# Performance work log

Hardware: AMD Instinct MI355X
Metric: run time of the kernel (lower is better)

The kernel has to match this reference:

```python
import jax, jax.numpy as jnp
import numpy as np
from jax.scipy.linalg import expm

B, S, D, E, K, NROT = 2, 2048, 1024, 8, 2, 3
EPS = 1e-5


def setup_inputs() -> dict:
    key = jax.random.key(0)
    ks = jax.random.split(key, 16)
    sc = 0.02
    x = jax.random.normal(ks[0], (B, S, D), jnp.float32)
    ln_gamma = 1.0 + sc * jax.random.normal(ks[1], (D,), jnp.float32)
    ln_beta = sc * jax.random.normal(ks[2], (D,), jnp.float32)
    abel_w = sc * jax.random.normal(ks[3], (D, D), jnp.float32)
    abel_b = sc * jax.random.normal(ks[4], (D,), jnp.float32)
    moe_gate_w = sc * jax.random.normal(ks[5], (D, E), jnp.float32)
    moe_gate_b = sc * jax.random.normal(ks[6], (E,), jnp.float32)
    ew1 = sc * jax.random.normal(ks[7], (E, D, 2 * D), jnp.float32)
    eb1 = sc * jax.random.normal(ks[8], (E, 2 * D), jnp.float32)
    ew2 = sc * jax.random.normal(ks[9], (E, 2 * D, D), jnp.float32)
    eb2 = sc * jax.random.normal(ks[10], (E, D), jnp.float32)
    g = sc * jax.random.normal(ks[11], (NROT, D, D), jnp.float32)
    gens = 0.5 * (g - jnp.swapaxes(g, -1, -2))  # skew-symmetric, as in reset_parameters
    gc_w = sc * jax.random.normal(ks[12], (2 * D, 1), jnp.float32)
    gc_b = sc * jax.random.normal(ks[13], (1,), jnp.float32)
    return dict(x=x, ln_gamma=ln_gamma, ln_beta=ln_beta, abel_w=abel_w, abel_b=abel_b,
                moe_gate_w=moe_gate_w, moe_gate_b=moe_gate_b, ew1=ew1, eb1=eb1,
                ew2=ew2, eb2=eb2, gens=gens, gc_w=gc_w, gc_b=gc_b)


def _gelu(x):
    return jax.nn.gelu(x, approximate=False)  # torch nn.GELU default = exact erf


def _forward(x, ln_gamma, ln_beta, abel_w, abel_b, moe_gate_w, moe_gate_b,
             ew1, eb1, ew2, eb2, gens, gc_w, gc_b):
    residual = x
    # LayerNorm
    mu = jnp.mean(x, axis=-1, keepdims=True)
    var = jnp.mean((x - mu) ** 2, axis=-1, keepdims=True)
    xn = (x - mu) * jax.lax.rsqrt(var + EPS) * ln_gamma + ln_beta
    # abel branch: Linear + GELU
    abel_out = _gelu(xn @ abel_w + abel_b)
    # MoE: dense all-experts compute, masked by top-k softmax weights
    logits = xn @ moe_gate_w + moe_gate_b                      # [B,S,E]
    topw, topi = jax.lax.top_k(logits, K)                      # [B,S,K]
    topw = jax.nn.softmax(topw, axis=-1)
    w_dense = jnp.sum(jax.nn.one_hot(topi, E, dtype=xn.dtype) * topw[..., None], axis=-2)  # [B,S,E]
    h = _gelu(jnp.einsum('bsd,edh->ebsh', xn, ew1) + eb1[:, None, None, :])  # [E,B,S,2D]
    eo = jnp.einsum('ebsh,ehd->ebsd', h, ew2) + eb2[:, None, None, :]        # [E,B,S,D]
    moe_out = jnp.einsum('ebsd,bse->bsd', eo, w_dense)
    # GeometricRotation: sequential matrix_exp rotations
    for i in range(NROT):
        moe_out = moe_out @ expm(gens[i])
    # gated residual mix
    combined = jnp.concatenate([abel_out, moe_out], axis=-1)
    gate = jax.nn.sigmoid(combined @ gc_w + gc_b)              # [B,S,1]
    mixed = abel_out * (1.0 - gate) + moe_out * gate
    return residual + mixed


def reference(x, ln_gamma, ln_beta, abel_w, abel_b, moe_gate_w, moe_gate_b,
              ew1, eb1, ew2, eb2, gens, gc_w, gc_b):
    return _forward(x, ln_gamma, ln_beta, abel_w, abel_b, moe_gate_w, moe_gate_b,
                    ew1, eb1, ew2, eb2, gens, gc_w, gc_b)
```

## Files before the change

kernel.cpp:

```cpp
#include <hip/hip_runtime.h>
#include <hip/hip_bf16.h>
#include <cstdint>
#include <cstddef>

#define DD   1024
#define DD2  2048
#define EE   8
#define NTOK 4096
#define CAPR 9216
#define MAXT 72

typedef __bf16 bf16_t;
typedef __bf16 bf16x8 __attribute__((ext_vector_type(8)));
typedef __bf16 bf16x4 __attribute__((ext_vector_type(4)));
typedef float  f32x4v __attribute__((ext_vector_type(4)));

__device__ __forceinline__ float gelu_f(float v){
  const float t = v*(0.7978845608028654f + 0.0356774081f*v*v);
  const float u = __expf(2.0f*t);
  return __fdividef(v*u, 1.0f + u);
}

__device__ __forceinline__ void gload_lds16(const void* g, void* l){
  __builtin_amdgcn_global_load_lds(
    (const __attribute__((address_space(1))) unsigned int*)(uintptr_t)g,
    (__attribute__((address_space(3))) unsigned int*)(uintptr_t)l,
    16, 0, 0);
}

enum { EPI_GELU_F32=0, EPI_GELU_BF16=1, EPI_BIAS_BF16=2, EPI_SCALE_BF16=3,
       EPI_ADDV_BF16=4, EPI_BF16=5, EPI_F32=6 };

template<int BM,int BN,int EPI,bool TAB>
__global__ __launch_bounds__(256)
void gemm_bt(const bf16_t* __restrict__ A, const bf16_t* __restrict__ Bt,
             const int N, const int K, const int gx, const int gy, const int gz,
             const long sAz, const long sBz, const long sOz,
             const int* __restrict__ tileE, const int* __restrict__ tileR,
             const int* __restrict__ ntp, const int* __restrict__ offp,
             const float* __restrict__ bias, const long sBias,
             const float alpha,
             const bf16_t* __restrict__ addv,
             float* __restrict__ outF, bf16_t* __restrict__ outB)
{
  constexpr int BK = 64;
  constexpr int WM = BM/2, WN = BN/2;
  constexpr int FM = WM/16, FN = WN/16;
  constexpr int IA = BM/32, IB = BN/32;
  __shared__ alignas(16) bf16_t sA[2][BM*BK];
  __shared__ alignas(16) bf16_t sB[2][BN*BK];

  int bx, by, bz;
  if constexpr (TAB) {
    const int nwg = gx * gy;
    const int q = nwg >> 3, r = nwg & 7;
    const int k = blockIdx.x & 7, i = blockIdx.x >> 3;
    if (i >= q + (k < r ? 1 : 0)) return;
    const int l = k * q + (k < r ? k : r) + i;
    const int ti = l / gx; bx = l - ti*gx;
    if (ti >= ntp[0]) return;
    bz = tileE[ti];
    by = 0;
    const long ro = (long)offp[bz] + tileR[ti];
    A    += ro * (long)K;
    outB += ro * (long)N;
  } else {
    const int nwg = gx * gy * gz;
    const int q = nwg >> 3, r = nwg & 7;
    const int k = blockIdx.x & 7, i = blockIdx.x >> 3;
    if (i >= q + (k < r ? 1 : 0)) return;
    const int l = k * q + (k < r ? k : r) + i;
    bx = l % gx; const int t2 = l / gx; by = t2 % gy; bz = t2 / gy;
  }

  const int z = bz;
  const bf16_t* Bp = Bt + (size_t)z * sBz;
  float*  oF = outF;
  bf16_t* oB = outB;
  if constexpr (!TAB) {
    A += (size_t)z * sAz;
    if (oF) oF += (size_t)z * sOz;
    if (oB) oB += (size_t)z * sOz;
  }
  const float*  bp = bias ? bias + (size_t)z * sBias : nullptr;
  const bf16_t* vp = addv ? addv + (size_t)z * sOz   : nullptr;

  const int tid = threadIdx.x;
  const int wid = tid >> 6, lid = tid & 63;
  const int wr = wid >> 1, wc = wid & 1;
  const int brow = by * BM, bcol = bx * BN;
  const int sr = lid >> 3, sq = lid & 7;
  const int fr = lid & 15, fq = lid >> 4;

  f32x4v acc[FM][FN] = {};

  auto stage = [&](int buf, int kt) {
    #pragma unroll
    for (int i = 0; i < IA; i++) {
      const int ii = wid*IA + i;
      const int r  = ii*8 + sr;
      const int q  = sq ^ (r & 7);
      gload_lds16((const char*)A + ((size_t)(brow + r)*K + kt)*2 + q*16,
                  (char*)sA[buf] + ii*1024);
    }
    #pragma unroll
    for (int i = 0; i < IB; i++) {
      const int ii = wid*IB + i;
      const int r  = ii*8 + sr;
      const int q  = sq ^ (r & 7);
      gload_lds16((const char*)Bp + ((size_t)(bcol + r)*K + kt)*2 + q*16,
                  (char*)sB[buf] + ii*1024);
    }
  };

  stage(0, 0);
  __syncthreads();
  int cur = 0;

  for (int kt = 0; kt < K; kt += BK) {
    if (kt + BK < K) stage(cur ^ 1, kt + BK);
    #pragma unroll
    for (int kk = 0; kk < 2; kk++) {
      bf16x8 af[FM], bb[FN];
      #pragma unroll
      for (int mi = 0; mi < FM; mi++) {
        const int r = wr*WM + mi*16 + fr;
        const int q = (kk*4 + fq) ^ (r & 7);
        af[mi] = *(const bf16x8*)((const char*)sA[cur] + r*128 + q*16);
      }
      #pragma unroll
      for (int ni = 0; ni < FN; ni++) {
        const int r = wc*WN + ni*16 + fr;
        const int q = (kk*4 + fq) ^ (r & 7);
        bb[ni] = *(const bf16x8*)((const char*)sB[cur] + r*128 + q*16);
      }
      #pragma unroll
      for (int mi = 0; mi < FM; mi++)
        #pragma unroll
        for (int ni = 0; ni < FN; ni++)
          acc[mi][ni] = __builtin_amdgcn_mfma_f32_16x16x32_bf16(
              af[mi], bb[ni], acc[mi][ni], 0, 0, 0);
    }
    __syncthreads();
    cur ^= 1;
  }

  #pragma unroll
  for (int mi = 0; mi < FM; mi++) {
    #pragma unroll
    for (int ni = 0; ni < FN; ni++) {
      const int rg0 = brow + wr*WM + mi*16 + fq*4;
      const int cg  = bcol + wc*WN + ni*16 + fr;
      #pragma unroll
      for (int i = 0; i < 4; i++) {
        const int rg = rg0 + i;
        float v = acc[mi][ni][i];
        if constexpr (EPI == EPI_GELU_F32) {
          v += bp[cg];
          oF[(size_t)rg*N + cg] = gelu_f(v);
        } else if constexpr (EPI == EPI_GELU_BF16) {
          v += bp[cg];
          oB[(size_t)rg*N + cg] = (bf16_t)gelu_f(v);
        } else if constexpr (EPI == EPI_BIAS_BF16) {
          v += bp[cg];
          oB[(size_t)rg*N + cg] = (bf16_t)v;
        } else if constexpr (EPI == EPI_SCALE_BF16) {
          oB[(size_t)rg*N + cg] = (bf16_t)(v * alpha);
        } else if constexpr (EPI == EPI_ADDV_BF16) {
          oB[(size_t)rg*N + cg] = (bf16_t)(v + (float)vp[(size_t)rg*N + cg]);
        } else if constexpr (EPI == EPI_BF16) {
          oB[(size_t)rg*N + cg] = (bf16_t)v;
        } else {
          oF[(size_t)rg*N + cg] = v;
        }
      }
    }
  }
}

__global__ __launch_bounds__(256)
void tcvt_kernel(const float* __restrict__ src, bf16_t* __restrict__ dst, int R, int C){
  __shared__ float t[64][65];
  const size_t bo = (size_t)blockIdx.z * R * C;
  const int c0 = blockIdx.x*64, r0 = blockIdx.y*64;
  const int lx = threadIdx.x & 15, ly = threadIdx.x >> 4;
  #pragma unroll
  for (int i = 0; i < 4; i++) {
    const int row = r0 + ly + i*16;
    const float4 v = *(const float4*)(src + bo + (size_t)row*C + c0 + lx*4);
    t[ly + i*16][lx*4+0] = v.x; t[ly + i*16][lx*4+1] = v.y;
    t[ly + i*16][lx*4+2] = v.z; t[ly + i*16][lx*4+3] = v.w;
  }
  __syncthreads();
  #pragma unroll
  for (int i = 0; i < 4; i++) {
    const int c = c0 + ly + i*16;
    bf16x4 o;
    #pragma unroll
    for (int j = 0; j < 4; j++) o[j] = (bf16_t)t[lx*4+j][ly + i*16];
    *(bf16x4*)(dst + bo + (size_t)c*R + r0 + lx*4) = o;
  }
}

__global__ __launch_bounds__(256)
void tb16_kernel(const bf16_t* __restrict__ Ut, bf16_t* __restrict__ Tb){
  __shared__ bf16_t tile[32][33];
  const bf16_t* src = Ut + (size_t)(1 - blockIdx.z) * DD * DD;
  bf16_t*       dst = Tb + (size_t)blockIdx.z * DD * DD;
  const int c0 = blockIdx.x*32, r0 = blockIdx.y*32;
  #pragma unroll
  for (int i = 0; i < 4; i++)
    tile[threadIdx.y + i*8][threadIdx.x] = src[(size_t)(r0 + threadIdx.y + i*8)*DD + c0 + threadIdx.x];
  __syncthreads();
  #pragma unroll
  for (int i = 0; i < 4; i++)
    dst[(size_t)(c0 + threadIdx.y + i*8)*DD + r0 + threadIdx.x] = tile[threadIdx.x][threadIdx.y + i*8];
}

__global__ __launch_bounds__(256)
void cvt_kernel(const float* __restrict__ in, bf16_t* __restrict__ o, long n, float scale){
  const long i = ((long)blockIdx.x*256 + threadIdx.x)*4;
  if (i >= n) return;
  const float4 v = *(const float4*)(in + i);
  bf16x4 b; b[0]=(bf16_t)(v.x*scale); b[1]=(bf16_t)(v.y*scale);
  b[2]=(bf16_t)(v.z*scale); b[3]=(bf16_t)(v.w*scale);
  *(bf16x4*)(o + i) = b;
}

__global__ __launch_bounds__(256)
void vw_kernel(const bf16_t* __restrict__ Hn, const bf16_t* __restrict__ H2,
               bf16_t* __restrict__ Vb, bf16_t* __restrict__ Wtb){
  const long i0 = ((long)blockIdx.x*256 + threadIdx.x)*4;
  const long rc = i0 % (long)(DD*DD);
  const int r = (int)(rc / DD), c0 = (int)(rc % DD);
  const bf16x4 h  = *(const bf16x4*)(Hn + i0);
  const bf16x4 h2 = *(const bf16x4*)(H2 + i0);
  bf16x4 v, w;
  #pragma unroll
  for (int j = 0; j < 4; j++) {
    const float d  = (r == c0 + j) ? 1.0f : 0.0f;
    const float fh = (float)h[j], f2 = (float)h2[j];
    v[j] = (bf16_t)(d + fh + f2*0.5f);
    w[j] = (bf16_t)(d*(1.0f/6.0f) - fh*(1.0f/24.0f) + f2*(1.0f/120.0f));
  }
  *(bf16x4*)(Vb  + i0) = v;
  *(bf16x4*)(Wtb + i0) = w;
}

__global__ __launch_bounds__(256)
void ln_gate_kernel(const float* __restrict__ x, const float* __restrict__ gamma,
                    const float* __restrict__ beta, const float* __restrict__ gw,
                    const float* __restrict__ gb,
                    bf16_t* __restrict__ xnb, int2* __restrict__ ids,
                    float2* __restrict__ wts)
{
  const int t = blockIdx.x, tid = threadIdx.x, j0 = tid*4;
  const int wid = tid >> 6, lid = tid & 63;
  const float4 v = *(const float4*)(x + (size_t)t*DD + j0);
  float s  = v.x + v.y + v.z + v.w;
  float ss = v.x*v.x + v.y*v.y + v.z*v.z + v.w*v.w;
  #pragma unroll
  for (int off = 32; off; off >>= 1) { s += __shfl_down(s, off); ss += __shfl_down(ss, off); }
  __shared__ float redS[4], redQ[4], mv[2];
  if (lid == 0) { redS[wid] = s; redQ[wid] = ss; }
  __syncthreads();
  if (tid == 0) {
    const float S1 = redS[0]+redS[1]+redS[2]+redS[3];
    const float S2 = redQ[0]+redQ[1]+redQ[2]+redQ[3];
    const float mu  = S1 * (1.0f/DD);
    const float var = S2 * (1.0f/DD) - mu*mu;
    mv[0] = mu; mv[1] = rsqrtf(var + 1e-5f);
  }
  __syncthreads();
  const float mu = mv[0], rstd = mv[1];
  const float4 g = *(const float4*)(gamma + j0);
  const float4 b = *(const float4*)(beta  + j0);
  float xn[4];
  xn[0] = (v.x-mu)*rstd*g.x + b.x;
  xn[1] = (v.y-mu)*rstd*g.y + b.y;
  xn[2] = (v.z-mu)*rstd*g.z + b.z;
  xn[3] = (v.w-mu)*rstd*g.w + b.w;
  bf16x4 ov; ov[0]=(bf16_t)xn[0]; ov[1]=(bf16_t)xn[1]; ov[2]=(bf16_t)xn[2]; ov[3]=(bf16_t)xn[3];
  *(bf16x4*)(xnb + (size_t)t*DD + j0) = ov;

  float p[8] = {0,0,0,0,0,0,0,0};
  #pragma unroll
  for (int i = 0; i < 4; i++) {
    const float4 a0 = *(const float4*)(gw + (size_t)(j0+i)*EE);
    const float4 a1 = *(const float4*)(gw + (size_t)(j0+i)*EE + 4);
    const float xv = xn[i];
    p[0]+=xv*a0.x; p[1]+=xv*a0.y; p[2]+=xv*a0.z; p[3]+=xv*a0.w;
    p[4]+=xv*a1.x; p[5]+=xv*a1.y; p[6]+=xv*a1.z; p[7]+=xv*a1.w;
  }
  #pragma unroll
  for (int off = 32; off; off >>= 1) {
    #pragma unroll
    for (int e = 0; e < 8; e++) p[e] += __shfl_down(p[e], off);
  }
  __shared__ float pr[32];
  if (lid == 0) {
    #pragma unroll
    for (int e = 0; e < 8; e++) pr[wid*8 + e] = p[e];
  }
  __syncthreads();
  if (tid == 0) {
    float l[8];
    #pragma unroll
    for (int e = 0; e < 8; e++) l[e] = pr[e] + pr[8+e] + pr[16+e] + pr[24+e] + gb[e];
    int i1 = 0; float m1 = l[0];
    #pragma unroll
    for (int e = 1; e < 8; e++) if (l[e] > m1) { m1 = l[e]; i1 = e; }
    int i2 = 0; float m2 = -1e30f;
    #pragma unroll
    for (int e = 0; e < 8; e++) if (e != i1 && l[e] > m2) { m2 = l[e]; i2 = e; }
    const float wa = 1.0f/(1.0f + expf(m2 - m1));
    ids[t] = make_int2(i1, i2);
    wts[t] = make_float2(wa, 1.0f - wa);
  }
}

__global__ __launch_bounds__(256)
void route_kernel(const int2* __restrict__ ids, int* __restrict__ slotA,
                  int* __restrict__ slotB, int* __restrict__ cnt,
                  int* __restrict__ off, int* __restrict__ tileE,
                  int* __restrict__ tileR, int* __restrict__ ntp)
{
  const int tid = threadIdx.x;
  const int wid = tid >> 6, lid = tid & 63;
  __shared__ int wsum[EE][4];
  __shared__ int base[EE];
  if (tid < EE) base[tid] = 0;
  __syncthreads();
  const unsigned long long lt = (1ull << lid) - 1ull;
  for (int c0 = 0; c0 < NTOK; c0 += 256) {
    const int t = c0 + tid;
    const int2 id = ids[t];
    int pA = 0, pB = 0;
    #pragma unroll
    for (int e = 0; e < EE; e++) {
      const bool fA = (id.x == e), fB = (id.y == e);
      const unsigned long long mA = __ballot(fA);
      const unsigned long long mB = __ballot(fB);
      const int cA = __popcll(mA);
      if (lid == 0) wsum[e][wid] = cA + __popcll(mB);
      if (fA) pA = __popcll(mA & lt);
      if (fB) pB = cA + __popcll(mB & lt);
    }
    __syncthreads();
    int wbA = base[id.x], wbB = base[id.y];
    for (int w = 0; w < wid; w++) { wbA += wsum[id.x][w]; wbB += wsum[id.y][w]; }
    slotA[t] = wbA + pA;
    slotB[t] = wbB + pB;
    __syncthreads();
    if (tid < EE) base[tid] += wsum[tid][0]+wsum[tid][1]+wsum[tid][2]+wsum[tid][3];
    __syncthreads();
  }
  if (tid == 0) {
    int a = 0, nt = 0;
    for (int e = 0; e < EE; e++) {
      cnt[e] = base[e]; off[e] = a;
      for (int r2 = 0; r2 < base[e]; r2 += 128) { tileE[nt] = e; tileR[nt] = r2; nt++; }
      a += (base[e] + 127) & ~127;
    }
    ntp[0] = nt;
  }
}

__global__ __launch_bounds__(256)
void gather_kernel(const bf16_t* __restrict__ xnb, const int2* __restrict__ ids,
                   const int* __restrict__ slotA, const int* __restrict__ slotB,
                   const int* __restrict__ off, bf16_t* __restrict__ Xg){
  const int t = blockIdx.x, j = threadIdx.x*4;
  const int2 id = ids[t];
  const bf16x4 v = *(const bf16x4*)(xnb + (size_t)t*DD + j);
  *(bf16x4*)(Xg + (size_t)(off[id.x] + slotA[t])*DD + j) = v;
  *(bf16x4*)(Xg + (size_t)(off[id.y] + slotB[t])*DD + j) = v;
}

__global__ __launch_bounds__(256)
void combine_kernel(const bf16_t* __restrict__ Yg, const int2* __restrict__ ids,
                    const int* __restrict__ slotA, const int* __restrict__ slotB,
                    const int* __restrict__ off, const float2* __restrict__ wts,
                    bf16_t* __restrict__ Xa){
  const int t = blockIdx.x, j = threadIdx.x*4;
  const int2 id = ids[t];
  const float2 w = wts[t];
  const bf16x4 a = *(const bf16x4*)(Yg + (size_t)(off[id.x] + slotA[t])*DD + j);
  const bf16x4 b = *(const bf16x4*)(Yg + (size_t)(off[id.y] + slotB[t])*DD + j);
  bf16x4 o;
  #pragma unroll
  for (int i = 0; i < 4; i++) o[i] = (bf16_t)(w.x*(float)a[i] + w.y*(float)b[i]);
  *(bf16x4*)(Xa + (size_t)t*DD + j) = o;
}

__global__ __launch_bounds__(256)
void mix_kernel(const float* __restrict__ x, const bf16_t* __restrict__ abel,
                const float* __restrict__ rot, const float* __restrict__ gcw,
                const float* __restrict__ gcb, float* __restrict__ out)
{
  const int t = blockIdx.x, tid = threadIdx.x, j0 = tid*4;
  const int wid = tid >> 6, lid = tid & 63;
  const bf16x4 ab = *(const bf16x4*)(abel + (size_t)t*DD + j0);
  const float4 r  = *(const float4*)(rot  + (size_t)t*DD + j0);
  const float4 ga = *(const float4*)(gcw + j0);
  const float4 gr = *(const float4*)(gcw + DD + j0);
  const float a0 = (float)ab[0], a1 = (float)ab[1], a2 = (float)ab[2], a3 = (float)ab[3];
  float p = a0*ga.x + a1*ga.y + a2*ga.z + a3*ga.w
          + r.x*gr.x + r.y*gr.y + r.z*gr.z + r.w*gr.w;
  #pragma unroll
  for (int off = 32; off; off >>= 1) p += __shfl_down(p, off);
  __shared__ float red[4];
  __shared__ float gsh;
  if (lid == 0) red[wid] = p;
  __syncthreads();
  if (tid == 0) {
    const float P = red[0] + red[1] + red[2] + red[3] + gcb[0];
    gsh = 1.0f/(1.0f + expf(-P));
  }
  __syncthreads();
  const float gate = gsh, g1 = 1.0f - gate;
  const float4 xv = *(const float4*)(x + (size_t)t*DD + j0);
  float4 o;
  o.x = xv.x + a0*g1 + r.x*gate;
  o.y = xv.y + a1*g1 + r.y*gate;
  o.z = xv.z + a2*g1 + r.z*gate;
  o.w = xv.w + a3*g1 + r.w*gate;
  *(float4*)(out + (size_t)t*DD + j0) = o;
}

extern "C" void kernel_launch(void* const* d_in, const int* in_sizes, int n_in,
                              void* d_out, int out_size, void* d_ws, size_t ws_size,
                              hipStream_t stream)
{
  (void)in_sizes; (void)n_in; (void)out_size; (void)ws_size;
  const float* x      = (const float*)d_in[0];
  const float* ln_g   = (const float*)d_in[1];
  const float* ln_b   = (const float*)d_in[2];
  const float* abel_w = (const float*)d_in[3];
  const float* abel_b = (const float*)d_in[4];
  const float* gate_w = (const float*)d_in[5];
  const float* gate_b = (const float*)d_in[6];
  const float* ew1    = (const float*)d_in[7];
  const float* eb1    = (const float*)d_in[8];
  const float* ew2    = (const float*)d_in[9];
  const float* eb2    = (const float*)d_in[10];
  const float* gens   = (const float*)d_in[11];
  const float* gc_w   = (const float*)d_in[12];
  const float* gc_b   = (const float*)d_in[13];
  float* out = (float*)d_out;

  char* wsp = (char*)d_ws;
  auto alloc = [&](size_t bytes) -> char* {
    char* p = wsp; wsp += (bytes + 255) & ~(size_t)255; return p;
  };
  const size_t MB = 1u<<20;
  bf16_t* xnb   = (bf16_t*)alloc((size_t)NTOK*DD*2);
  int2*   ids   = (int2*)  alloc((size_t)NTOK*8);
  float2* wts   = (float2*)alloc((size_t)NTOK*8);
  int*    slotA = (int*)   alloc((size_t)NTOK*4);
  int*    slotB = (int*)   alloc((size_t)NTOK*4);
  int*    cnt   = (int*)   alloc(64);
  int*    off   = (int*)   alloc(64);
  int*    tileE = (int*)   alloc(MAXT*4);
  int*    tileR = (int*)   alloc(MAXT*4);
  int*    ntp   = (int*)   alloc(64);
  bf16_t* abel_wT = (bf16_t*)alloc((size_t)DD*DD*2);
  char*   UN      = alloc(64*MB);
  bf16_t* ew1T  = (bf16_t*)UN;
  bf16_t* ew2T  = (bf16_t*)(UN + 32*MB);
  bf16_t* Hn    = (bf16_t*)alloc((size_t)3*DD*DD*2);
  bf16_t* abelo = (bf16_t*)alloc((size_t)NTOK*DD*2);
  bf16_t* Xg    = (bf16_t*)alloc((size_t)CAPR*DD*2);
  bf16_t* Hg    = (bf16_t*)alloc((size_t)CAPR*DD2*2);
  bf16_t* Xa    = (bf16_t*)alloc((size_t)NTOK*DD*2);
  bf16_t* Yg    = Xg;
  float*  rot   = (float*)Hg;
  bf16_t* H2  = (bf16_t*)(UN + 0*MB);
  bf16_t* H3  = (bf16_t*)(UN + 6*MB);
  bf16_t* Vb  = (bf16_t*)(UN + 12*MB);
  bf16_t* Wtb = (bf16_t*)(UN + 18*MB);
  bf16_t* Ut  = (bf16_t*)(UN + 24*MB);
  bf16_t* Tb  = (bf16_t*)(UN + 30*MB);
  bf16_t* Pb  = (bf16_t*)(UN + 34*MB);
  bf16_t* Rt  = (bf16_t*)(UN + 36*MB);
  const long D2 = (long)DD*DD;

  auto gflat = [](int gx, int gy, int gz) {
    const int nwg = gx*gy*gz; return 8 * ((nwg + 7) / 8);
  };

  tcvt_kernel<<<dim3(DD/64,  DD/64, 1),  256, 0, stream>>>(abel_w, abel_wT, DD,  DD);
  tcvt_kernel<<<dim3(DD2/64, DD/64, EE), 256, 0, stream>>>(ew1,    ew1T,    DD,  DD2);
  tcvt_kernel<<<dim3(DD/64,  DD2/64,EE), 256, 0, stream>>>(ew2,    ew2T,    DD2, DD);
  cvt_kernel<<<dim3(3*DD*DD/1024,1,1), 256, 0, stream>>>(gens, Hn, (long)3*DD*DD, -1.0f);

  ln_gate_kernel<<<dim3(NTOK,1,1), 256, 0, stream>>>(x, ln_g, ln_b, gate_w, gate_b,
                                                     xnb, ids, wts);
  route_kernel<<<dim3(1,1,1), 256, 0, stream>>>(ids, slotA, slotB, cnt, off,
                                                tileE, tileR, ntp);
  gather_kernel<<<dim3(NTOK,1,1), 256, 0, stream>>>(xnb, ids, slotA, slotB, off, Xg);

  gemm_bt<128,128,EPI_GELU_BF16,true><<<dim3((DD2/128)*MAXT,1,1), 256, 0, stream>>>(
      Xg, ew1T, DD2, DD, DD2/128, MAXT, 1, 0, (long)DD2*DD, 0,
      tileE, tileR, ntp, off, eb1, DD2, 1.0f, nullptr, nullptr, Hg);
  gemm_bt<128,128,EPI_BIAS_BF16,true><<<dim3((DD/128)*MAXT,1,1), 256, 0, stream>>>(
      Hg, ew2T, DD, DD2, DD/128, MAXT, 1, 0, (long)DD*DD2, 0,
      tileE, tileR, ntp, off, eb2, DD, 1.0f, nullptr, nullptr, Yg);
  combine_kernel<<<dim3(NTOK,1,1), 256, 0, stream>>>(Yg, ids, slotA, slotB, off, wts, Xa);

  gemm_bt<128,64,EPI_GELU_BF16,false><<<dim3(gflat(16,32,1),1,1), 256, 0, stream>>>(
      xnb, abel_wT, DD, DD, 16, 32, 1, 0, 0, 0, nullptr, nullptr, nullptr, nullptr,
      abel_b, 0, 1.0f, nullptr, nullptr, abelo);

  gemm_bt<128,64,EPI_SCALE_BF16,false><<<dim3(gflat(16,8,3),1,1), 256, 0, stream>>>(
      Hn, Hn, DD, DD, 16, 8, 3, D2, D2, D2, nullptr, nullptr, nullptr, nullptr,
      nullptr, 0, -1.0f, nullptr, nullptr, H2);
  gemm_bt<128,64,EPI_SCALE_BF16,false><<<dim3(gflat(16,8,3),1,1), 256, 0, stream>>>(
      H2, Hn, DD, DD, 16, 8, 3, D2, D2, D2, nullptr, nullptr, nullptr, nullptr,
      nullptr, 0, -1.0f, nullptr, nullptr, H3);
  vw_kernel<<<dim3(3*DD*DD/1024,1,1), 256, 0, stream>>>(Hn, H2, Vb, Wtb);
  gemm_bt<128,64,EPI_ADDV_BF16,false><<<dim3(gflat(16,8,3),1,1), 256, 0, stream>>>(
      H3, Wtb, DD, DD, 16, 8, 3, D2, D2, D2, nullptr, nullptr, nullptr, nullptr,
      nullptr, 0, 1.0f, Vb, nullptr, Ut);
  tb16_kernel<<<dim3(32,32,2), dim3(32,8,1), 0, stream>>>(Ut, Tb);
  gemm_bt<64,64,EPI_BF16,false><<<dim3(gflat(16,16,1),1,1), 256, 0, stream>>>(
      Ut + 2*D2, Tb, DD, DD, 16, 16, 1, 0, 0, 0, nullptr, nullptr, nullptr, nullptr,
      nullptr, 0, 1.0f, nullptr, nullptr, Pb);
  gemm_bt<64,64,EPI_BF16,false><<<dim3(gflat(16,16,1),1,1), 256, 0, stream>>>(
      Pb, Tb + D2, DD, DD, 16, 16, 1, 0, 0, 0, nullptr, nullptr, nullptr, nullptr,
      nullptr, 0, 1.0f, nullptr, nullptr, Rt);
  gemm_bt<128,64,EPI_F32,false><<<dim3(gflat(16,32,1),1,1), 256, 0, stream>>>(
      Xa, Rt, DD, DD, 16, 32, 1, 0, 0, 0, nullptr, nullptr, nullptr, nullptr,
      nullptr, 0, 1.0f, nullptr, rot, nullptr);

  mix_kernel<<<dim3(NTOK,1,1), 256, 0, stream>>>(x, abelo, rot, gc_w, gc_b, out);
}
```

Measured before the change: 342.8 us.

## Triple-buffer GEMM with BK=32, fuse MoE gather into GEMM loads, enlarge tiles

The GEMM main loop moves from a double-buffered BK=64 scheme to a triple-buffered BK=32 pipeline with explicit vmcnt waits and one barrier per k-step, and precomputes per-thread source pointers. The first expert GEMM now reads token rows from the normalized input through a token-index table, so the gather kernel that materialized Xg is dropped and replaced by a small index fill plus a memset. Several dense GEMMs switch from 128x64 to 128x128 tiles. This removes a full copy of the routed activations and aims to hide load latency better, at the cost of smaller k-steps, fewer workgroups for the dense GEMMs, and indirect row addressing.

```diff
diff --git a/kernel.cpp b/kernel.cpp
--- a/kernel.cpp
+++ b/kernel.cpp
@@ -38,19 +38,21 @@
              const long sAz, const long sBz, const long sOz,
              const int* __restrict__ tileE, const int* __restrict__ tileR,
              const int* __restrict__ ntp, const int* __restrict__ offp,
+             const int* __restrict__ tokOf,
              const float* __restrict__ bias, const long sBias,
              const float alpha,
              const bf16_t* __restrict__ addv,
              float* __restrict__ outF, bf16_t* __restrict__ outB)
 {
-  constexpr int BK = 64;
+  constexpr int BK = 32;
   constexpr int WM = BM/2, WN = BN/2;
   constexpr int FM = WM/16, FN = WN/16;
-  constexpr int IA = BM/32, IB = BN/32;
-  __shared__ alignas(16) bf16_t sA[2][BM*BK];
-  __shared__ alignas(16) bf16_t sB[2][BN*BK];
-
-  int bx, by, bz;
+  constexpr int IA = BM/64, IB = BN/64;
+  constexpr int NLD = IA + IB;
+  __shared__ alignas(16) bf16_t sA[3][BM*BK];
+  __shared__ alignas(16) bf16_t sB[3][BN*BK];
+
+  int bx, by, bz; long ro = 0;
   if constexpr (TAB) {
     const int nwg = gx * gy;
     const int q = nwg >> 3, r = nwg & 7;
@@ -59,11 +61,8 @@
     const int l = k * q + (k < r ? k : r) + i;
     const int ti = l / gx; bx = l - ti*gx;
     if (ti >= ntp[0]) return;
-    bz = tileE[ti];
-    by = 0;
-    const long ro = (long)offp[bz] + tileR[ti];
-    A    += ro * (long)K;
-    outB += ro * (long)N;
+    bz = tileE[ti]; by = 0;
+    ro = (long)offp[bz] + tileR[ti];
   } else {
     const int nwg = gx * gy * gz;
     const int q = nwg >> 3, r = nwg & 7;
@@ -77,7 +76,9 @@
   const bf16_t* Bp = Bt + (size_t)z * sBz;
   float*  oF = outF;
   bf16_t* oB = outB;
-  if constexpr (!TAB) {
+  if constexpr (TAB) {
+    oB += ro * (long)N;
+  } else {
     A += (size_t)z * sAz;
     if (oF) oF += (size_t)z * sOz;
     if (oB) oB += (size_t)z * sOz;
@@ -89,60 +90,75 @@
   const int wid = tid >> 6, lid = tid & 63;
   const int wr = wid >> 1, wc = wid & 1;
   const int brow = by * BM, bcol = bx * BN;
-  const int sr = lid >> 3, sq = lid & 7;
   const int fr = lid & 15, fq = lid >> 4;
+  const int rl = lid >> 2, qs = lid & 3;
+
+  const char* aSrc[IA];
+  const char* bSrc[IB];
+  #pragma unroll
+  for (int i = 0; i < IA; i++) {
+    const int rloc = (wid*IA + i)*16 + rl;
+    const int q = qs ^ ((rloc >> 1) & 3);
+    const bf16_t* arow;
+    if constexpr (TAB) {
+      arow = tokOf ? (A + (size_t)tokOf[ro + rloc] * K)
+                   : (A + (size_t)(ro + rloc) * K);
+    } else {
+      arow = A + (size_t)(brow + rloc) * K;
+    }
+    aSrc[i] = (const char*)arow + q*16;
+  }
+  #pragma unroll
+  for (int i = 0; i < IB; i++) {
+    const int rloc = (wid*IB + i)*16 + rl;
+    const int q = qs ^ ((rloc >> 1) & 3);
+    bSrc[i] = (const char*)(Bp + (size_t)(bcol + rloc) * K) + q*16;
+  }
 
   f32x4v acc[FM][FN] = {};
 
   auto stage = [&](int buf, int kt) {
     #pragma unroll
-    for (int i = 0; i < IA; i++) {
-      const int ii = wid*IA + i;
-      const int r  = ii*8 + sr;
-      const int q  = sq ^ (r & 7);
-      gload_lds16((const char*)A + ((size_t)(brow + r)*K + kt)*2 + q*16,
-                  (char*)sA[buf] + ii*1024);
+    for (int i = 0; i < IA; i++)
+      gload_lds16(aSrc[i] + (size_t)kt*2, (char*)sA[buf] + (wid*IA + i)*1024);
+    #pragma unroll
+    for (int i = 0; i < IB; i++)
+      gload_lds16(bSrc[i] + (size_t)kt*2, (char*)sB[buf] + (wid*IB + i)*1024);
+  };
+
+  stage(0, 0);
+  stage(1, BK);
+  const int nk = K / BK;
+  int b0 = 0, b1 = 1, b2 = 2;
+
+  for (int t = 0; t < nk; ++t) {
+    if (t < nk - 1) asm volatile("s_waitcnt vmcnt(%0)" :: "i"(NLD) : "memory");
+    else            asm volatile("s_waitcnt vmcnt(0)" ::: "memory");
+    __builtin_amdgcn_s_barrier();
+    __builtin_amdgcn_sched_barrier(0);
+    if (t + 2 < nk) stage(b2, (t + 2)*BK);
+
+    bf16x8 af[FM], bb[FN];
+    #pragma unroll
+    for (int mi = 0; mi < FM; mi++) {
+      const int r2 = wr*WM + mi*16 + fr;
+      const int q = fq ^ ((r2 >> 1) & 3);
+      af[mi] = *(const bf16x8*)((const char*)sA[b0] + r2*64 + q*16);
     }
     #pragma unroll
-    for (int i = 0; i < IB; i++) {
-      const int ii = wid*IB + i;
-      const int r  = ii*8 + sr;
-      const int q  = sq ^ (r & 7);
-      gload_lds16((const char*)Bp + ((size_t)(bcol + r)*K + kt)*2 + q*16,
-                  (char*)sB[buf] + ii*1024);
+    for (int ni = 0; ni < FN; ni++) {
+      const int r2 = wc*WN + ni*16 + fr;
+      const int q = fq ^ ((r2 >> 1) & 3);
+      bb[ni] = *(const bf16x8*)((const char*)sB[b0] + r2*64 + q*16);
     }
-  };
-
-  stage(0, 0);
-  __syncthreads();
-  int cur = 0;
-
-  for (int kt = 0; kt < K; kt += BK) {
-    if (kt + BK < K) stage(cur ^ 1, kt + BK);
-    #pragma unroll
-    for (int kk = 0; kk < 2; kk++) {
-      bf16x8 af[FM], bb[FN];
+    #pragma unroll
+    for (int mi = 0; mi < FM; mi++)
       #pragma unroll
-      for (int mi = 0; mi < FM; mi++) {
-        const int r = wr*WM + mi*16 + fr;
-        const int q = (kk*4 + fq) ^ (r & 7);
-        af[mi] = *(const bf16x8*)((const char*)sA[cur] + r*128 + q*16);
-      }
-      #pragma unroll
-      for (int ni = 0; ni < FN; ni++) {
-        const int r = wc*WN + ni*16 + fr;
-        const int q = (kk*4 + fq) ^ (r & 7);
-        bb[ni] = *(const bf16x8*)((const char*)sB[cur] + r*128 + q*16);
-      }
-      #pragma unroll
-      for (int mi = 0; mi < FM; mi++)
-        #pragma unroll
-        for (int ni = 0; ni < FN; ni++)
-          acc[mi][ni] = __builtin_amdgcn_mfma_f32_16x16x32_bf16(
-              af[mi], bb[ni], acc[mi][ni], 0, 0, 0);
-    }
-    __syncthreads();
-    cur ^= 1;
+      for (int ni = 0; ni < FN; ni++)
+        acc[mi][ni] = __builtin_amdgcn_mfma_f32_16x16x32_bf16(
+            af[mi], bb[ni], acc[mi][ni], 0, 0, 0);
+
+    const int tb_ = b0; b0 = b1; b1 = b2; b2 = tb_;
   }
 
   #pragma unroll
@@ -367,14 +383,13 @@
 }
 
 __global__ __launch_bounds__(256)
-void gather_kernel(const bf16_t* __restrict__ xnb, const int2* __restrict__ ids,
-                   const int* __restrict__ slotA, const int* __restrict__ slotB,
-                   const int* __restrict__ off, bf16_t* __restrict__ Xg){
-  const int t = blockIdx.x, j = threadIdx.x*4;
+void fill_tok_kernel(const int2* __restrict__ ids, const int* __restrict__ slotA,
+                     const int* __restrict__ slotB, const int* __restrict__ off,
+                     int* __restrict__ tokOf){
+  const int t = blockIdx.x*256 + threadIdx.x;
   const int2 id = ids[t];
-  const bf16x4 v = *(const bf16x4*)(xnb + (size_t)t*DD + j);
-  *(bf16x4*)(Xg + (size_t)(off[id.x] + slotA[t])*DD + j) = v;
-  *(bf16x4*)(Xg + (size_t)(off[id.y] + slotB[t])*DD + j) = v;
+  tokOf[off[id.x] + slotA[t]] = t;
+  tokOf[off[id.y] + slotB[t]] = t;
 }
 
 __global__ __launch_bounds__(256)
@@ -464,16 +479,16 @@
   int*    tileE = (int*)   alloc(MAXT*4);
   int*    tileR = (int*)   alloc(MAXT*4);
   int*    ntp   = (int*)   alloc(64);
+  int*    tokOf = (int*)   alloc((size_t)CAPR*4);
   bf16_t* abel_wT = (bf16_t*)alloc((size_t)DD*DD*2);
   char*   UN      = alloc(64*MB);
   bf16_t* ew1T  = (bf16_t*)UN;
   bf16_t* ew2T  = (bf16_t*)(UN + 32*MB);
   bf16_t* Hn    = (bf16_t*)alloc((size_t)3*DD*DD*2);
   bf16_t* abelo = (bf16_t*)alloc((size_t)NTOK*DD*2);
-  bf16_t* Xg    = (bf16_t*)alloc((size_t)CAPR*DD*2);
+  bf16_t* Yg    = (bf16_t*)alloc((size_t)CAPR*DD*2);
   bf16_t* Hg    = (bf16_t*)alloc((size_t)CAPR*DD2*2);
   bf16_t* Xa    = (bf16_t*)alloc((size_t)NTOK*DD*2);
-  bf16_t* Yg    = Xg;
   float*  rot   = (float*)Hg;
   bf16_t* H2  = (bf16_t*)(UN + 0*MB);
   bf16_t* H3  = (bf16_t*)(UN + 6*MB);
@@ -493,45 +508,46 @@
   tcvt_kernel<<<dim3(DD2/64, DD/64, EE), 256, 0, stream>>>(ew1,    ew1T,    DD,  DD2);
   tcvt_kernel<<<dim3(DD/64,  DD2/64,EE), 256, 0, stream>>>(ew2,    ew2T,    DD2, DD);
   cvt_kernel<<<dim3(3*DD*DD/1024,1,1), 256, 0, stream>>>(gens, Hn, (long)3*DD*DD, -1.0f);
+  hipMemsetAsync(tokOf, 0, (size_t)CAPR*4, stream);
 
   ln_gate_kernel<<<dim3(NTOK,1,1), 256, 0, stream>>>(x, ln_g, ln_b, gate_w, gate_b,
                                                      xnb, ids, wts);
   route_kernel<<<dim3(1,1,1), 256, 0, stream>>>(ids, slotA, slotB, cnt, off,
                                                 tileE, tileR, ntp);
-  gather_kernel<<<dim3(NTOK,1,1), 256, 0, stream>>>(xnb, ids, slotA, slotB, off, Xg);
+  fill_tok_kernel<<<dim3(NTOK/256,1,1), 256, 0, stream>>>(ids, slotA, slotB, off, tokOf);
 
   gemm_bt<128,128,EPI_GELU_BF16,true><<<dim3((DD2/128)*MAXT,1,1), 256, 0, stream>>>(
-      Xg, ew1T, DD2, DD, DD2/128, MAXT, 1, 0, (long)DD2*DD, 0,
-      tileE, tileR, ntp, off, eb1, DD2, 1.0f, nullptr, nullptr, Hg);
+      xnb, ew1T, DD2, DD, DD2/128, MAXT, 1, 0, (long)DD2*DD, 0,
+      tileE, tileR, ntp, off, tokOf, eb1, DD2, 1.0f, nullptr, nullptr, Hg);
   gemm_bt<128,128,EPI_BIAS_BF16,true><<<dim3((DD/128)*MAXT,1,1), 256, 0, stream>>>(
       Hg, ew2T, DD, DD2, DD/128, MAXT, 1, 0, (long)DD*DD2, 0,
-      tileE, tileR, ntp, off, eb2, DD, 1.0f, nullptr, nullptr, Yg);
+      tileE, tileR, ntp, off, nullptr, eb2, DD, 1.0f, nullptr, nullptr, Yg);
   combine_kernel<<<dim3(NTOK,1,1), 256, 0, stream>>>(Yg, ids, slotA, slotB, off, wts, Xa);
 
-  gemm_bt<128,64,EPI_GELU_BF16,false><<<dim3(gflat(16,32,1),1,1), 256, 0, stream>>>(
-      xnb, abel_wT, DD, DD, 16, 32, 1, 0, 0, 0, nullptr, nullptr, nullptr, nullptr,
-      abel_b, 0, 1.0f, nullptr, nullptr, abelo);
-
-  gemm_bt<128,64,EPI_SCALE_BF16,false><<<dim3(gflat(16,8,3),1,1), 256, 0, stream>>>(
-      Hn, Hn, DD, DD, 16, 8, 3, D2, D2, D2, nullptr, nullptr, nullptr, nullptr,
-      nullptr, 0, -1.0f, nullptr, nullptr, H2);
-  gemm_bt<128,64,EPI_SCALE_BF16,false><<<dim3(gflat(16,8,3),1,1), 256, 0, stream>>>(
-      H2, Hn, DD, DD, 16, 8, 3, D2, D2, D2, nullptr, nullptr, nullptr, nullptr,
-      nullptr, 0, -1.0f, nullptr, nullptr, H3);
+  gemm_bt<128,128,EPI_GELU_BF16,false><<<dim3(gflat(8,32,1),1,1), 256, 0, stream>>>(
+      xnb, abel_wT, DD, DD, 8, 32, 1, 0, 0, 0, nullptr, nullptr, nullptr, nullptr,
+      nullptr, abel_b, 0, 1.0f, nullptr, nullptr, abelo);
+
+  gemm_bt<128,128,EPI_SCALE_BF16,false><<<dim3(gflat(8,8,3),1,1), 256, 0, stream>>>(
+      Hn, Hn, DD, DD, 8, 8, 3, D2, D2, D2, nullptr, nullptr, nullptr, nullptr,
+      nullptr, nullptr, 0, -1.0f, nullptr, nullptr, H2);
+  gemm_bt<128,128,EPI_SCALE_BF16,false><<<dim3(gflat(8,8,3),1,1), 256, 0, stream>>>(
+      H2, Hn, DD, DD, 8, 8, 3, D2, D2, D2, nullptr, nullptr, nullptr, nullptr,
+      nullptr, nullptr, 0, -1.0f, nullptr, nullptr, H3);
   vw_kernel<<<dim3(3*DD*DD/1024,1,1), 256, 0, stream>>>(Hn, H2, Vb, Wtb);
-  gemm_bt<128,64,EPI_ADDV_BF16,false><<<dim3(gflat(16,8,3),1,1), 256, 0, stream>>>(
-      H3, Wtb, DD, DD, 16, 8, 3, D2, D2, D2, nullptr, nullptr, nullptr, nullptr,
-      nullptr, 0, 1.0f, Vb, nullptr, Ut);
+  gemm_bt<128,128,EPI_ADDV_BF16,false><<<dim3(gflat(8,8,3),1,1), 256, 0, stream>>>(
+      H3, Wtb, DD, DD, 8, 8, 3, D2, D2, D2, nullptr, nullptr, nullptr, nullptr,
+      nullptr, nullptr, 0, 1.0f, Vb, nullptr, Ut);
   tb16_kernel<<<dim3(32,32,2), dim3(32,8,1), 0, stream>>>(Ut, Tb);
   gemm_bt<64,64,EPI_BF16,false><<<dim3(gflat(16,16,1),1,1), 256, 0, stream>>>(
       Ut + 2*D2, Tb, DD, DD, 16, 16, 1, 0, 0, 0, nullptr, nullptr, nullptr, nullptr,
-      nullptr, 0, 1.0f, nullptr, nullptr, Pb);
+      nullptr, nullptr, 0, 1.0f, nullptr, nullptr, Pb);
   gemm_bt<64,64,EPI_BF16,false><<<dim3(gflat(16,16,1),1,1), 256, 0, stream>>>(
       Pb, Tb + D2, DD, DD, 16, 16, 1, 0, 0, 0, nullptr, nullptr, nullptr, nullptr,
-      nullptr, 0, 1.0f, nullptr, nullptr, Rt);
-  gemm_bt<128,64,EPI_F32,false><<<dim3(gflat(16,32,1),1,1), 256, 0, stream>>>(
-      Xa, Rt, DD, DD, 16, 32, 1, 0, 0, 0, nullptr, nullptr, nullptr, nullptr,
-      nullptr, 0, 1.0f, nullptr, rot, nullptr);
+      nullptr, nullptr, 0, 1.0f, nullptr, nullptr, Rt);
+  gemm_bt<128,128,EPI_F32,false><<<dim3(gflat(8,32,1),1,1), 256, 0, stream>>>(
+      Xa, Rt, DD, DD, 8, 32, 1, 0, 0, 0, nullptr, nullptr, nullptr, nullptr,
+      nullptr, nullptr, 0, 1.0f, nullptr, rot, nullptr);
 
   mix_kernel<<<dim3(NTOK,1,1), 256, 0, stream>>>(x, abelo, rot, gc_w, gc_b, out);
 }
```

After: 339.1 us. No clear change (-1.1%).
